# Performance work log

Hardware: AMD Instinct MI355X
Metric: run time of the kernel (lower is better)

## Reference

```python
import jax, jax.numpy as jnp
import numpy as np

N_NEURONS = 50000
N_EDGES = 1600000
EMB_DIM = 2
HID = 128


def _mlp3(x, w0, b0, w1, b1, w2, b2):
    # 3-layer MLP with tanh activations between linear layers (tanh MLP_activation)
    h = jnp.tanh(x @ w0 + b0)
    h = jnp.tanh(h @ w1 + b1)
    return h @ w2 + b2


def setup_inputs() -> dict:
    key = jax.random.key(0)
    ks = jax.random.split(key, 16)
    v = jax.random.normal(ks[0], (N_NEURONS, 1), dtype=jnp.float32)
    excitation = jax.random.uniform(ks[1], (N_NEURONS, 1), dtype=jnp.float32)
    edge_src = jax.random.randint(ks[2], (N_EDGES,), 0, N_NEURONS)
    edge_dst = jax.random.randint(ks[3], (N_EDGES,), 0, N_NEURONS)
    # learnable node embedding a (init ones in torch code; use ones + small noise for generality)
    a = jnp.ones((N_NEURONS, EMB_DIM), jnp.float32) + 0.01 * jax.random.normal(ks[4], (N_NEURONS, EMB_DIM), dtype=jnp.float32)
    # per-edge connectivity W, shape (E, 1) (w_init_mode='randn_scaled')
    W = jax.random.normal(ks[5], (N_EDGES, 1), dtype=jnp.float32) / np.sqrt(N_EDGES).astype(np.float32)
    def lin(k, fan_in, fan_out):
        bound = 1.0 / np.sqrt(fan_in)
        kw, kb = jax.random.split(k)
        w = jax.random.uniform(kw, (fan_in, fan_out), jnp.float32, -bound, bound)
        b = jax.random.uniform(kb, (fan_out,), jnp.float32, -bound, bound)
        return w, b
    # g_phi: input (v_j, a_j) -> 3 dims -> HID -> HID -> 1
    g0_w, g0_b = lin(ks[6], 1 + EMB_DIM, HID)
    g1_w, g1_b = lin(ks[7], HID, HID)
    g2_w, g2_b = lin(ks[8], HID, 1)
    # f_theta: input (v, a, msg, excitation) -> 5 dims -> HID -> HID -> 1
    f0_w, f0_b = lin(ks[9], 1 + EMB_DIM + 1 + 1, HID)
    f1_w, f1_b = lin(ks[10], HID, HID)
    f2_w, f2_b = lin(ks[11], HID, 1)
    return {"v": v, "excitation": excitation, "edge_src": edge_src, "edge_dst": edge_dst,
            "a": a, "W": W,
            "g0_w": g0_w, "g0_b": g0_b, "g1_w": g1_w, "g1_b": g1_b, "g2_w": g2_w, "g2_b": g2_b,
            "f0_w": f0_w, "f0_b": f0_b, "f1_w": f1_w, "f1_b": f1_b, "f2_w": f2_w, "f2_b": f2_b}


def reference(v, excitation, edge_src, edge_dst, a, W,
              g0_w, g0_b, g1_w, g1_b, g2_w, g2_b,
              f0_w, f0_b, f1_w, f1_b, f2_w, f2_b):
    # --- edge messages (flyvis_A): msg_e = W[e] * g_phi(v_src, a_src)^2 ---
    edge_in = jnp.concatenate([v[edge_src], a[edge_src]], axis=1)          # (E, 3)
    g = _mlp3(edge_in, g0_w, g0_b, g1_w, g1_b, g2_w, g2_b)                 # (E, 1)
    msg_e = W * jnp.square(g)                                              # (E, 1), g_phi_positive
    # --- scatter_add aggregation into destination nodes ---
    msg = jax.ops.segment_sum(msg_e, edge_dst, num_segments=N_NEURONS)     # (N, 1)
    # --- node update: du/dt = f_theta(v, a, msg, excitation) ---
    node_in = jnp.concatenate([v, a, msg, excitation], axis=1)             # (N, 5)
    dudt = _mlp3(node_in, f0_w, f0_b, f1_w, f1_b, f2_w, f2_b)              # (N, 1)
    return dudt
```

## Files before the change

### kernel.cpp

```cpp
#include <hip/hip_runtime.h>
#include <hip/hip_bf16.h>

#define HID   128
#define NPB   64
#define PITCH 136
#define CH0   32768

#define FRAGN 16384

typedef float f32x4  __attribute__((ext_vector_type(4)));
typedef short bf16x8 __attribute__((ext_vector_type(8)));

__device__ __forceinline__ float fast_tanh(float x) {
    const float e = __expf(2.0f * x);
    return 1.0f - 2.0f / (e + 1.0f);
}

__device__ __forceinline__ short f2bf(float x) {
    union { __hip_bfloat16 h; short s; } u;
    u.h = __float2bfloat16(x);
    return u.s;
}

__global__ __launch_bounds__(256) void prep_kernel(
    const float* __restrict__ g1_w, const float* __restrict__ g1_b, const float* __restrict__ g2_w,
    const float* __restrict__ f1_w, const float* __restrict__ f1_b, const float* __restrict__ f2_w,
    short* __restrict__ gfrag, short* __restrict__ ffrag,
    float* __restrict__ gbw, float* __restrict__ fbw)
{
    const int id  = blockIdx.x * 256 + threadIdx.x;
    const int mat = (id >= 2560);
    const int r   = id - (mat ? 2560 : 0);
    const float* __restrict__ w1 = mat ? f1_w : g1_w;
    const float* __restrict__ b1 = mat ? f1_b : g1_b;
    const float* __restrict__ w2 = mat ? f2_w : g2_w;
    short* __restrict__ frag = mat ? ffrag : gfrag;
    float* __restrict__ bw   = mat ? fbw   : gbw;

    if (r < 2048) {
        const int j16  = r >> 8;
        const int s    = (r >> 6) & 3;
        const int lane = r & 63;
        const int m = lane & 15, kg = lane >> 4;
        const int j  = j16 * 16 + m;
        const int k0 = 32 * s + 8 * kg;
        bf16x8 f;
#pragma unroll
        for (int e = 0; e < 8; ++e) f[e] = f2bf(w1[(k0 + e) * HID + j]);
        *(bf16x8*)&frag[r * 8] = f;
    } else if (r < 2560) {
        const int q = r - 2048;
        const int j16 = q >> 6, lane = q & 63, kg = lane >> 4;
#pragma unroll
        for (int rr = 0; rr < 4; ++rr) {
            bw[q * 8 + rr]     = b1[j16 * 16 + 4 * kg + rr];
            bw[q * 8 + 4 + rr] = w2[j16 * 16 + 4 * kg + rr];
        }
    }
}

__global__ __launch_bounds__(256) void node_g_kernel(
    const float* __restrict__ v, const float* __restrict__ a,
    const float* __restrict__ g0_w, const float* __restrict__ g0_b,
    const short* __restrict__ gfrag, const float* __restrict__ gbw,
    const float* __restrict__ g2_b,
    float* __restrict__ gsq, int N)
{
    const int t    = threadIdx.x;
    const int lane = t & 63;
    const int wq   = t >> 6;
    const int base = blockIdx.x * NPB;
    const int m    = lane & 15;
    const int kg   = lane >> 4;

    __shared__ __align__(16) __hip_bfloat16 h0bf[NPB * PITCH];
    __shared__ float xv[NPB];
    __shared__ float xa[2 * NPB];
    __shared__ float red[4][4][16];

    if (t < NPB) {
        int node = base + t; if (node >= N) node = N - 1;
        xv[t] = v[node];
    } else if (t >= 128) {
        int idx = 2 * base + (t - 128);
        const int lim = 2 * N - 1; if (idx > lim) idx = lim;
        xa[t - 128] = a[idx];
    }

    bf16x8 afrag[2][4];
    float b1v[2][4], w2v[2][4];
    const bf16x8* __restrict__ fb = (const bf16x8*)gfrag;
#pragma unroll
    for (int jt = 0; jt < 2; ++jt) {
        const int j16 = 2 * wq + jt;
#pragma unroll
        for (int s = 0; s < 4; ++s)
            afrag[jt][s] = fb[(j16 * 4 + s) * 64 + lane];
        const f32x4 bv = *(const f32x4*)&gbw[(j16 * 64 + lane) * 8];
        const f32x4 wv = *(const f32x4*)&gbw[(j16 * 64 + lane) * 8 + 4];
#pragma unroll
        for (int r = 0; r < 4; ++r) { b1v[jt][r] = bv[r]; w2v[jt][r] = wv[r]; }
    }
    __syncthreads();

    {
        const int j    = t & 127;
        const int half = t >> 7;
        const float w00 = g0_w[0 * HID + j];
        const float w01 = g0_w[1 * HID + j];
        const float w02 = g0_w[2 * HID + j];
        const float b0  = g0_b[j];
#pragma unroll 4
        for (int i = 0; i < 32; ++i) {
            const int nn = half * 32 + i;
            h0bf[nn * PITCH + j] = __float2bfloat16(
                fast_tanh(b0 + xv[nn] * w00 + xa[2 * nn] * w01 + xa[2 * nn + 1] * w02));
        }
    }
    __syncthreads();

#pragma unroll
    for (int nt = 0; nt < 4; ++nt) {
        const int n = nt * 16 + m;
        f32x4 acc0 = {0.f, 0.f, 0.f, 0.f};
        f32x4 acc1 = {0.f, 0.f, 0.f, 0.f};
#pragma unroll
        for (int s = 0; s < 4; ++s) {
            const bf16x8 b = *(const bf16x8*)&h0bf[n * PITCH + 32 * s + 8 * kg];
            acc0 = __builtin_amdgcn_mfma_f32_16x16x32_bf16(afrag[0][s], b, acc0, 0, 0, 0);
            acc1 = __builtin_amdgcn_mfma_f32_16x16x32_bf16(afrag[1][s], b, acc1, 0, 0, 0);
        }
        float p = 0.f;
#pragma unroll
        for (int r = 0; r < 4; ++r) {
            p += w2v[0][r] * fast_tanh(acc0[r] + b1v[0][r]);
            p += w2v[1][r] * fast_tanh(acc1[r] + b1v[1][r]);
        }
        p += __shfl_down(p, 32);
        p += __shfl_down(p, 16);
        if (lane < 16) red[wq][nt][lane] = p;
    }
    __syncthreads();

    if (t < NPB) {
        const int node = base + t;
        if (node < N) {
            const float g = red[0][t >> 4][t & 15] + red[1][t >> 4][t & 15]
                          + red[2][t >> 4][t & 15] + red[3][t >> 4][t & 15]
                          + g2_b[0];
            gsq[node] = g * g;
        }
    }
}

__global__ __launch_bounds__(256) void edge_kernel(
    const int* __restrict__ src, const int* __restrict__ dst,
    const float* __restrict__ W, const float* __restrict__ gsq,
    float* __restrict__ partial, int B, int N, int E)
{
    __shared__ float loc[CH0];
    const int t = threadIdx.x;
    const int p = blockIdx.x >> 1;
    const int c = blockIdx.x & 1;

    const f32x4 z4 = {0.f, 0.f, 0.f, 0.f};
    for (int i = 4 * t; i < CH0; i += 1024) *(f32x4*)&loc[i] = z4;
    __syncthreads();

    int cnt = (E + B - 1) / B;
    cnt = (cnt + 3) & ~3;
    const int start = p * cnt;
    int end = start + cnt; if (end > E) end = E;
    const int coff = c << 15;

    if (start < end) {
        const int nvec = (end - start) & ~3;
        for (int i = 4 * t; i < nvec; i += 1024) {
            const int e = start + i;
            const int4   s4 = *(const int4*)&src[e];
            const int4   d4 = *(const int4*)&dst[e];
            const float4 w4 = *(const float4*)&W[e];
            if ((d4.x >> 15) == c) atomicAdd(&loc[d4.x - coff], w4.x * gsq[s4.x]);
            if ((d4.y >> 15) == c) atomicAdd(&loc[d4.y - coff], w4.y * gsq[s4.y]);
            if ((d4.z >> 15) == c) atomicAdd(&loc[d4.z - coff], w4.z * gsq[s4.z]);
            if ((d4.w >> 15) == c) atomicAdd(&loc[d4.w - coff], w4.w * gsq[s4.w]);
        }
        for (int e = start + nvec + t; e < end; e += 256) {
            const int d = dst[e];
            if ((d >> 15) == c) atomicAdd(&loc[d - coff], W[e] * gsq[src[e]]);
        }
    }
    __syncthreads();

    int chN = c ? (N - CH0) : CH0; if (chN > CH0) chN = CH0;
    float* __restrict__ dp = partial + (size_t)p * N + coff;
    const int chV = chN & ~3;
    for (int i = 4 * t; i < chV; i += 1024) *(f32x4*)&dp[i] = *(const f32x4*)&loc[i];
    for (int i = chV + t; i < chN; i += 256) dp[i] = loc[i];
}

__global__ __launch_bounds__(256) void node_f_kernel(
    const float* __restrict__ v, const float* __restrict__ a,
    const float* __restrict__ exc, const float* __restrict__ partial, int B,
    const float* __restrict__ f0_w, const float* __restrict__ f0_b,
    const short* __restrict__ ffrag, const float* __restrict__ fbw,
    const float* __restrict__ f2_b,
    float* __restrict__ out, int N)
{
    const int t    = threadIdx.x;
    const int lane = t & 63;
    const int wq   = t >> 6;
    const int base = blockIdx.x * NPB;
    const int m    = lane & 15;
    const int kg   = lane >> 4;

    __shared__ __align__(16) __hip_bfloat16 h0bf[NPB * PITCH];
    __shared__ float xv[NPB];
    __shared__ float xe[NPB];
    __shared__ float xa[2 * NPB];
    __shared__ float xm4[4][NPB];
    __shared__ float red[4][4][16];

    if (t < NPB) {
        int node = base + t; if (node >= N) node = N - 1;
        xv[t] = v[node];
    } else if (t < 128) {
        int node = base + (t - 64); if (node >= N) node = N - 1;
        xe[t - 64] = exc[node];
    } else {
        int idx = 2 * base + (t - 128);
        const int lim = 2 * N - 1; if (idx > lim) idx = lim;
        xa[t - 128] = a[idx];
    }
    {
        const int n16 = t & 63, grp = t >> 6;
        int node = base + n16; if (node >= N) node = N - 1;
        const int pb = B >> 2;
        float s = 0.f;
        for (int p = grp * pb; p < (grp + 1) * pb; ++p)
            s += partial[(size_t)p * N + node];
        xm4[grp][n16] = s;
    }

    bf16x8 afrag[2][4];
    float b1v[2][4], w2v[2][4];
    const bf16x8* __restrict__ fb = (const bf16x8*)ffrag;
#pragma unroll
    for (int jt = 0; jt < 2; ++jt) {
        const int j16 = 2 * wq + jt;
#pragma unroll
        for (int s = 0; s < 4; ++s)
            afrag[jt][s] = fb[(j16 * 4 + s) * 64 + lane];
        const f32x4 bv = *(const f32x4*)&fbw[(j16 * 64 + lane) * 8];
        const f32x4 wv = *(const f32x4*)&fbw[(j16 * 64 + lane) * 8 + 4];
#pragma unroll
        for (int r = 0; r < 4; ++r) { b1v[jt][r] = bv[r]; w2v[jt][r] = wv[r]; }
    }
    __syncthreads();

    {
        const int j    = t & 127;
        const int half = t >> 7;
        const float w00 = f0_w[0 * HID + j];
        const float w01 = f0_w[1 * HID + j];
        const float w02 = f0_w[2 * HID + j];
        const float w03 = f0_w[3 * HID + j];
        const float w04 = f0_w[4 * HID + j];
        const float b0  = f0_b[j];
#pragma unroll 4
        for (int i = 0; i < 32; ++i) {
            const int nn = half * 32 + i;
            const float x3 = (xm4[0][nn] + xm4[1][nn]) + (xm4[2][nn] + xm4[3][nn]);
            h0bf[nn * PITCH + j] = __float2bfloat16(
                fast_tanh(b0 + xv[nn] * w00 + xa[2 * nn] * w01 + xa[2 * nn + 1] * w02
                             + x3 * w03 + xe[nn] * w04));
        }
    }
    __syncthreads();

#pragma unroll
    for (int nt = 0; nt < 4; ++nt) {
        const int n = nt * 16 + m;
        f32x4 acc0 = {0.f, 0.f, 0.f, 0.f};
        f32x4 acc1 = {0.f, 0.f, 0.f, 0.f};
#pragma unroll
        for (int s = 0; s < 4; ++s) {
            const bf16x8 b = *(const bf16x8*)&h0bf[n * PITCH + 32 * s + 8 * kg];
            acc0 = __builtin_amdgcn_mfma_f32_16x16x32_bf16(afrag[0][s], b, acc0, 0, 0, 0);
            acc1 = __builtin_amdgcn_mfma_f32_16x16x32_bf16(afrag[1][s], b, acc1, 0, 0, 0);
        }
        float p = 0.f;
#pragma unroll
        for (int r = 0; r < 4; ++r) {
            p += w2v[0][r] * fast_tanh(acc0[r] + b1v[0][r]);
            p += w2v[1][r] * fast_tanh(acc1[r] + b1v[1][r]);
        }
        p += __shfl_down(p, 32);
        p += __shfl_down(p, 16);
        if (lane < 16) red[wq][nt][lane] = p;
    }
    __syncthreads();

    if (t < NPB) {
        const int node = base + t;
        if (node < N) {
            out[node] = red[0][t >> 4][t & 15] + red[1][t >> 4][t & 15]
                      + red[2][t >> 4][t & 15] + red[3][t >> 4][t & 15]
                      + f2_b[0];
        }
    }
}

extern "C" void kernel_launch(void* const* d_in, const int* in_sizes, int n_in,
                              void* d_out, int out_size, void* d_ws, size_t ws_size,
                              hipStream_t stream)
{
    const float* v    = (const float*)d_in[0];
    const float* exc  = (const float*)d_in[1];
    const int*   esrc = (const int*)d_in[2];
    const int*   edst = (const int*)d_in[3];
    const float* a    = (const float*)d_in[4];
    const float* W    = (const float*)d_in[5];
    const float* g0_w = (const float*)d_in[6];
    const float* g0_b = (const float*)d_in[7];
    const float* g1_w = (const float*)d_in[8];
    const float* g1_b = (const float*)d_in[9];
    const float* g2_w = (const float*)d_in[10];
    const float* g2_b = (const float*)d_in[11];
    const float* f0_w = (const float*)d_in[12];
    const float* f0_b = (const float*)d_in[13];
    const float* f1_w = (const float*)d_in[14];
    const float* f1_b = (const float*)d_in[15];
    const float* f2_w = (const float*)d_in[16];
    const float* f2_b = (const float*)d_in[17];

    const int N = in_sizes[0];
    const int E = in_sizes[2];

    int B = 128;
    while (B > 4 && (size_t)(1 + B) * (size_t)N * sizeof(float) + 131072 > ws_size) B >>= 1;

    float* gsq     = (float*)d_ws;
    float* partial = gsq + N;
    short* gfrag   = (short*)(partial + (size_t)B * N);
    short* ffrag   = gfrag + FRAGN;
    float* gbw     = (float*)(ffrag + FRAGN);
    float* fbw     = gbw + 4096;

    const int nblocks = (N + NPB - 1) / NPB;

    prep_kernel<<<20, 256, 0, stream>>>(g1_w, g1_b, g2_w, f1_w, f1_b, f2_w,
                                        gfrag, ffrag, gbw, fbw);

    node_g_kernel<<<nblocks, 256, 0, stream>>>(v, a, g0_w, g0_b,
                                               gfrag, gbw, g2_b, gsq, N);

    edge_kernel<<<2 * B, 256, 0, stream>>>(esrc, edst, W, gsq, partial, B, N, E);

    node_f_kernel<<<nblocks, 256, 0, stream>>>(v, a, exc, partial, B,
                                               f0_w, f0_b, ffrag, fbw, f2_b,
                                               (float*)d_out, N);
}
```

Measured before the change: 157.1 us.

## Fuse all four stages into one cooperative persistent kernel with grid syncs

```diff
diff --git a/kernel.cpp b/kernel.cpp
--- a/kernel.cpp
+++ b/kernel.cpp
@@ -1,12 +1,17 @@
 #include <hip/hip_runtime.h>
 #include <hip/hip_bf16.h>
-
-#define HID   128
-#define NPB   64
-#define PITCH 136
-#define CH0   32768
-
-#define FRAGN 16384
+#include <hip/hip_cooperative_groups.h>
+
+namespace cg = cooperative_groups;
+
+#define HID    128
+#define NPB    64
+#define PITCH  136
+#define CH0    32768
+#define BLOCKS 256
+#define TPB    1024
+#define BPARTS 128
+#define FRAGN  16384
 
 typedef float f32x4  __attribute__((ext_vector_type(4)));
 typedef short bf16x8 __attribute__((ext_vector_type(8)));
@@ -15,298 +20,295 @@
     const float e = __expf(2.0f * x);
     return 1.0f - 2.0f / (e + 1.0f);
 }
-
 __device__ __forceinline__ short f2bf(float x) {
     union { __hip_bfloat16 h; short s; } u;
     u.h = __float2bfloat16(x);
     return u.s;
 }
 
-__global__ __launch_bounds__(256) void prep_kernel(
-    const float* __restrict__ g1_w, const float* __restrict__ g1_b, const float* __restrict__ g2_w,
-    const float* __restrict__ f1_w, const float* __restrict__ f1_b, const float* __restrict__ f2_w,
-    short* __restrict__ gfrag, short* __restrict__ ffrag,
-    float* __restrict__ gbw, float* __restrict__ fbw)
+__global__ __launch_bounds__(TPB) void fused_kernel(
+    const float* __restrict__ v, const float* __restrict__ exc,
+    const int* __restrict__ esrc, const int* __restrict__ edst,
+    const float* __restrict__ a, const float* __restrict__ W,
+    const float* __restrict__ g0_w, const float* __restrict__ g0_b,
+    const float* __restrict__ g1_w, const float* __restrict__ g1_b,
+    const float* __restrict__ g2_w, const float* __restrict__ g2_b,
+    const float* __restrict__ f0_w, const float* __restrict__ f0_b,
+    const float* __restrict__ f1_w, const float* __restrict__ f1_b,
+    const float* __restrict__ f2_w, const float* __restrict__ f2_b,
+    float* __restrict__ out, float* __restrict__ ws, int N, int E)
 {
-    const int id  = blockIdx.x * 256 + threadIdx.x;
-    const int mat = (id >= 2560);
-    const int r   = id - (mat ? 2560 : 0);
-    const float* __restrict__ w1 = mat ? f1_w : g1_w;
-    const float* __restrict__ b1 = mat ? f1_b : g1_b;
-    const float* __restrict__ w2 = mat ? f2_w : g2_w;
-    short* __restrict__ frag = mat ? ffrag : gfrag;
-    float* __restrict__ bw   = mat ? fbw   : gbw;
-
-    if (r < 2048) {
-        const int j16  = r >> 8;
-        const int s    = (r >> 6) & 3;
-        const int lane = r & 63;
-        const int m = lane & 15, kg = lane >> 4;
-        const int j  = j16 * 16 + m;
-        const int k0 = 32 * s + 8 * kg;
-        bf16x8 f;
-#pragma unroll
-        for (int e = 0; e < 8; ++e) f[e] = f2bf(w1[(k0 + e) * HID + j]);
-        *(bf16x8*)&frag[r * 8] = f;
-    } else if (r < 2560) {
-        const int q = r - 2048;
-        const int j16 = q >> 6, lane = q & 63, kg = lane >> 4;
-#pragma unroll
-        for (int rr = 0; rr < 4; ++rr) {
-            bw[q * 8 + rr]     = b1[j16 * 16 + 4 * kg + rr];
-            bw[q * 8 + 4 + rr] = w2[j16 * 16 + 4 * kg + rr];
-        }
-    }
-}
-
-__global__ __launch_bounds__(256) void node_g_kernel(
-    const float* __restrict__ v, const float* __restrict__ a,
-    const float* __restrict__ g0_w, const float* __restrict__ g0_b,
-    const short* __restrict__ gfrag, const float* __restrict__ gbw,
-    const float* __restrict__ g2_b,
-    float* __restrict__ gsq, int N)
-{
-    const int t    = threadIdx.x;
+    float* gsq     = ws;
+    float* partial = ws + N;
+    short* gfrag   = (short*)(partial + (size_t)BPARTS * N);
+    short* ffrag   = gfrag + FRAGN;
+    float* gbw     = (float*)(ffrag + FRAGN);
+    float* fbw     = gbw + 4096;
+
+    cg::grid_group grid = cg::this_grid();
+
+    __shared__ __align__(16) char lds[131072];
+
+    const int tid  = threadIdx.x;
+    const int team = tid >> 8;
+    const int t    = tid & 255;
     const int lane = t & 63;
     const int wq   = t >> 6;
-    const int base = blockIdx.x * NPB;
     const int m    = lane & 15;
     const int kg   = lane >> 4;
-
-    __shared__ __align__(16) __hip_bfloat16 h0bf[NPB * PITCH];
-    __shared__ float xv[NPB];
-    __shared__ float xa[2 * NPB];
-    __shared__ float red[4][4][16];
-
-    if (t < NPB) {
-        int node = base + t; if (node >= N) node = N - 1;
-        xv[t] = v[node];
-    } else if (t >= 128) {
-        int idx = 2 * base + (t - 128);
-        const int lim = 2 * N - 1; if (idx > lim) idx = lim;
-        xa[t - 128] = a[idx];
+    const int tile = blockIdx.x * 4 + team;
+    const int base = tile * NPB;
+
+    char* tb = lds + team * 32768;
+    __hip_bfloat16* h0bf = (__hip_bfloat16*)tb;
+    float* xv  = (float*)(tb + 17408);
+    float* xa  = (float*)(tb + 17664);
+    float* xe  = (float*)(tb + 18176);
+    float* xm4 = (float*)(tb + 18432);
+    float* red = (float*)(tb + 19456);
+
+    {
+        const int id = blockIdx.x * TPB + tid;
+        if (id < 5120) {
+            const int mat = (id >= 2560);
+            const int r   = id - (mat ? 2560 : 0);
+            const float* __restrict__ w1 = mat ? f1_w : g1_w;
+            const float* __restrict__ b1 = mat ? f1_b : g1_b;
+            const float* __restrict__ w2 = mat ? f2_w : g2_w;
+            short* __restrict__ frag = mat ? ffrag : gfrag;
+            float* __restrict__ bw   = mat ? fbw   : gbw;
+            if (r < 2048) {
+                const int j16 = r >> 8, s = (r >> 6) & 3, ln = r & 63;
+                const int mm = ln & 15, kk = ln >> 4;
+                const int j = j16 * 16 + mm, k0 = 32 * s + 8 * kk;
+                bf16x8 f;
+#pragma unroll
+                for (int e = 0; e < 8; ++e) f[e] = f2bf(w1[(k0 + e) * HID + j]);
+                *(bf16x8*)&frag[r * 8] = f;
+            } else if (r < 2560) {
+                const int q = r - 2048;
+                const int j16 = q >> 6, ln = q & 63, kk = ln >> 4;
+#pragma unroll
+                for (int rr = 0; rr < 4; ++rr) {
+                    bw[q * 8 + rr]     = b1[j16 * 16 + 4 * kk + rr];
+                    bw[q * 8 + 4 + rr] = w2[j16 * 16 + 4 * kk + rr];
+                }
+            }
+        }
     }
-
-    bf16x8 afrag[2][4];
-    float b1v[2][4], w2v[2][4];
-    const bf16x8* __restrict__ fb = (const bf16x8*)gfrag;
-#pragma unroll
-    for (int jt = 0; jt < 2; ++jt) {
-        const int j16 = 2 * wq + jt;
-#pragma unroll
-        for (int s = 0; s < 4; ++s)
-            afrag[jt][s] = fb[(j16 * 4 + s) * 64 + lane];
-        const f32x4 bv = *(const f32x4*)&gbw[(j16 * 64 + lane) * 8];
-        const f32x4 wv = *(const f32x4*)&gbw[(j16 * 64 + lane) * 8 + 4];
-#pragma unroll
-        for (int r = 0; r < 4; ++r) { b1v[jt][r] = bv[r]; w2v[jt][r] = wv[r]; }
+    grid.sync();
+
+    {
+        if (t < NPB) {
+            int node = base + t; if (node >= N) node = N - 1;
+            xv[t] = v[node];
+        } else if (t >= 128) {
+            int idx = 2 * base + (t - 128);
+            const int lim = 2 * N - 1; if (idx > lim) idx = lim;
+            xa[t - 128] = a[idx];
+        }
+
+        bf16x8 afrag[2][4];
+        float b1v[2][4], w2v[2][4];
+        const bf16x8* __restrict__ fb = (const bf16x8*)gfrag;
+#pragma unroll
+        for (int jt = 0; jt < 2; ++jt) {
+            const int j16 = 2 * wq + jt;
+#pragma unroll
+            for (int s = 0; s < 4; ++s)
+                afrag[jt][s] = fb[(j16 * 4 + s) * 64 + lane];
+            const f32x4 bv = *(const f32x4*)&gbw[(j16 * 64 + lane) * 8];
+            const f32x4 wv = *(const f32x4*)&gbw[(j16 * 64 + lane) * 8 + 4];
+#pragma unroll
+            for (int r = 0; r < 4; ++r) { b1v[jt][r] = bv[r]; w2v[jt][r] = wv[r]; }
+        }
+        __syncthreads();
+
+        {
+            const int j    = t & 127;
+            const int half = t >> 7;
+            const float w00 = g0_w[0 * HID + j];
+            const float w01 = g0_w[1 * HID + j];
+            const float w02 = g0_w[2 * HID + j];
+            const float b0  = g0_b[j];
+#pragma unroll 4
+            for (int i = 0; i < 32; ++i) {
+                const int nn = half * 32 + i;
+                h0bf[nn * PITCH + j] = __float2bfloat16(
+                    fast_tanh(b0 + xv[nn] * w00 + xa[2 * nn] * w01 + xa[2 * nn + 1] * w02));
+            }
+        }
+        __syncthreads();
+
+#pragma unroll
+        for (int nt = 0; nt < 4; ++nt) {
+            const int n = nt * 16 + m;
+            f32x4 acc0 = {0.f, 0.f, 0.f, 0.f};
+            f32x4 acc1 = {0.f, 0.f, 0.f, 0.f};
+#pragma unroll
+            for (int s = 0; s < 4; ++s) {
+                const bf16x8 b = *(const bf16x8*)&h0bf[n * PITCH + 32 * s + 8 * kg];
+                acc0 = __builtin_amdgcn_mfma_f32_16x16x32_bf16(afrag[0][s], b, acc0, 0, 0, 0);
+                acc1 = __builtin_amdgcn_mfma_f32_16x16x32_bf16(afrag[1][s], b, acc1, 0, 0, 0);
+            }
+            float p = 0.f;
+#pragma unroll
+            for (int r = 0; r < 4; ++r) {
+                p += w2v[0][r] * fast_tanh(acc0[r] + b1v[0][r]);
+                p += w2v[1][r] * fast_tanh(acc1[r] + b1v[1][r]);
+            }
+            p += __shfl_down(p, 32);
+            p += __shfl_down(p, 16);
+            if (lane < 16) red[(wq * 4 + nt) * 16 + lane] = p;
+        }
+        __syncthreads();
+
+        if (t < NPB) {
+            const int node = base + t;
+            if (node < N) {
+                const int nt = t >> 4, n16 = t & 15;
+                const float g = red[(0 * 4 + nt) * 16 + n16] + red[(1 * 4 + nt) * 16 + n16]
+                              + red[(2 * 4 + nt) * 16 + n16] + red[(3 * 4 + nt) * 16 + n16]
+                              + g2_b[0];
+                gsq[node] = g * g;
+            }
+        }
     }
-    __syncthreads();
+    grid.sync();
 
     {
-        const int j    = t & 127;
-        const int half = t >> 7;
-        const float w00 = g0_w[0 * HID + j];
-        const float w01 = g0_w[1 * HID + j];
-        const float w02 = g0_w[2 * HID + j];
-        const float b0  = g0_b[j];
+        float* __restrict__ loc = (float*)lds;
+        const int p = blockIdx.x >> 1;
+        const int c = blockIdx.x & 1;
+
+        const f32x4 z4 = {0.f, 0.f, 0.f, 0.f};
+        for (int i = 4 * tid; i < CH0; i += 4 * TPB) *(f32x4*)&loc[i] = z4;
+        __syncthreads();
+
+        int cnt = (E + BPARTS - 1) / BPARTS;
+        cnt = (cnt + 3) & ~3;
+        const int start = p * cnt;
+        int end = start + cnt; if (end > E) end = E;
+        const int coff = c << 15;
+
+        if (start < end) {
+            const int nvec = (end - start) & ~3;
+            for (int i = 4 * tid; i < nvec; i += 4 * TPB) {
+                const int e = start + i;
+                const int4   s4 = *(const int4*)&esrc[e];
+                const int4   d4 = *(const int4*)&edst[e];
+                const float4 w4 = *(const float4*)&W[e];
+                if ((d4.x >> 15) == c) atomicAdd(&loc[d4.x - coff], w4.x * gsq[s4.x]);
+                if ((d4.y >> 15) == c) atomicAdd(&loc[d4.y - coff], w4.y * gsq[s4.y]);
+                if ((d4.z >> 15) == c) atomicAdd(&loc[d4.z - coff], w4.z * gsq[s4.z]);
+                if ((d4.w >> 15) == c) atomicAdd(&loc[d4.w - coff], w4.w * gsq[s4.w]);
+            }
+            for (int e = start + nvec + tid; e < end; e += TPB) {
+                const int d = edst[e];
+                if ((d >> 15) == c) atomicAdd(&loc[d - coff], W[e] * gsq[esrc[e]]);
+            }
+        }
+        __syncthreads();
+
+        int chN = c ? (N - CH0) : CH0;
+        if (chN > CH0) chN = CH0; if (chN < 0) chN = 0;
+        float* __restrict__ dp = partial + (size_t)p * N + coff;
+        const int chV = chN & ~3;
+        for (int i = 4 * tid; i < chV; i += 4 * TPB) *(f32x4*)&dp[i] = *(const f32x4*)&loc[i];
+        for (int i = chV + tid; i < chN; i += TPB) dp[i] = loc[i];
+    }
+    grid.sync();
+
+    {
+        if (t < NPB) {
+            int node = base + t; if (node >= N) node = N - 1;
+            xv[t] = v[node];
+        } else if (t < 128) {
+            int node = base + (t - 64); if (node >= N) node = N - 1;
+            xe[t - 64] = exc[node];
+        } else {
+            int idx = 2 * base + (t - 128);
+            const int lim = 2 * N - 1; if (idx > lim) idx = lim;
+            xa[t - 128] = a[idx];
+        }
+        {
+            const int n16 = t & 63, grp = t >> 6;
+            int node = base + n16; if (node >= N) node = N - 1;
+            const int pb = BPARTS >> 2;
+            float s = 0.f;
+            for (int p = grp * pb; p < (grp + 1) * pb; ++p)
+                s += partial[(size_t)p * N + node];
+            xm4[grp * NPB + n16] = s;
+        }
+
+        bf16x8 afrag[2][4];
+        float b1v[2][4], w2v[2][4];
+        const bf16x8* __restrict__ fb = (const bf16x8*)ffrag;
+#pragma unroll
+        for (int jt = 0; jt < 2; ++jt) {
+            const int j16 = 2 * wq + jt;
+#pragma unroll
+            for (int s = 0; s < 4; ++s)
+                afrag[jt][s] = fb[(j16 * 4 + s) * 64 + lane];
+            const f32x4 bv = *(const f32x4*)&fbw[(j16 * 64 + lane) * 8];
+            const f32x4 wv = *(const f32x4*)&fbw[(j16 * 64 + lane) * 8 + 4];
+#pragma unroll
+            for (int r = 0; r < 4; ++r) { b1v[jt][r] = bv[r]; w2v[jt][r] = wv[r]; }
+        }
+        __syncthreads();
+
+        {
+            const int j    = t & 127;
+            const int half = t >> 7;
+            const float w00 = f0_w[0 * HID + j];
+            const float w01 = f0_w[1 * HID + j];
+            const float w02 = f0_w[2 * HID + j];
+            const float w03 = f0_w[3 * HID + j];
+            const float w04 = f0_w[4 * HID + j];
+            const float b0  = f0_b[j];
 #pragma unroll 4
-        for (int i = 0; i < 32; ++i) {
-            const int nn = half * 32 + i;
-            h0bf[nn * PITCH + j] = __float2bfloat16(
-                fast_tanh(b0 + xv[nn] * w00 + xa[2 * nn] * w01 + xa[2 * nn + 1] * w02));
-        }
-    }
-    __syncthreads();
-
-#pragma unroll
-    for (int nt = 0; nt < 4; ++nt) {
-        const int n = nt * 16 + m;
-        f32x4 acc0 = {0.f, 0.f, 0.f, 0.f};
-        f32x4 acc1 = {0.f, 0.f, 0.f, 0.f};
-#pragma unroll
-        for (int s = 0; s < 4; ++s) {
-            const bf16x8 b = *(const bf16x8*)&h0bf[n * PITCH + 32 * s + 8 * kg];
-            acc0 = __builtin_amdgcn_mfma_f32_16x16x32_bf16(afrag[0][s], b, acc0, 0, 0, 0);
-            acc1 = __builtin_amdgcn_mfma_f32_16x16x32_bf16(afrag[1][s], b, acc1, 0, 0, 0);
-        }
-        float p = 0.f;
-#pragma unroll
-        for (int r = 0; r < 4; ++r) {
-            p += w2v[0][r] * fast_tanh(acc0[r] + b1v[0][r]);
-            p += w2v[1][r] * fast_tanh(acc1[r] + b1v[1][r]);
-        }
-        p += __shfl_down(p, 32);
-        p += __shfl_down(p, 16);
-        if (lane < 16) red[wq][nt][lane] = p;
-    }
-    __syncthreads();
-
-    if (t < NPB) {
-        const int node = base + t;
-        if (node < N) {
-            const float g = red[0][t >> 4][t & 15] + red[1][t >> 4][t & 15]
-                          + red[2][t >> 4][t & 15] + red[3][t >> 4][t & 15]
-                          + g2_b[0];
-            gsq[node] = g * g;
-        }
-    }
-}
-
-__global__ __launch_bounds__(256) void edge_kernel(
-    const int* __restrict__ src, const int* __restrict__ dst,
-    const float* __restrict__ W, const float* __restrict__ gsq,
-    float* __restrict__ partial, int B, int N, int E)
-{
-    __shared__ float loc[CH0];
-    const int t = threadIdx.x;
-    const int p = blockIdx.x >> 1;
-    const int c = blockIdx.x & 1;
-
-    const f32x4 z4 = {0.f, 0.f, 0.f, 0.f};
-    for (int i = 4 * t; i < CH0; i += 1024) *(f32x4*)&loc[i] = z4;
-    __syncthreads();
-
-    int cnt = (E + B - 1) / B;
-    cnt = (cnt + 3) & ~3;
-    const int start = p * cnt;
-    int end = start + cnt; if (end > E) end = E;
-    const int coff = c << 15;
-
-    if (start < end) {
-        const int nvec = (end - start) & ~3;
-        for (int i = 4 * t; i < nvec; i += 1024) {
-            const int e = start + i;
-            const int4   s4 = *(const int4*)&src[e];
-            const int4   d4 = *(const int4*)&dst[e];
-            const float4 w4 = *(const float4*)&W[e];
-            if ((d4.x >> 15) == c) atomicAdd(&loc[d4.x - coff], w4.x * gsq[s4.x]);
-            if ((d4.y >> 15) == c) atomicAdd(&loc[d4.y - coff], w4.y * gsq[s4.y]);
-            if ((d4.z >> 15) == c) atomicAdd(&loc[d4.z - coff], w4.z * gsq[s4.z]);
-            if ((d4.w >> 15) == c) atomicAdd(&loc[d4.w - coff], w4.w * gsq[s4.w]);
-        }
-        for (int e = start + nvec + t; e < end; e += 256) {
-            const int d = dst[e];
-            if ((d >> 15) == c) atomicAdd(&loc[d - coff], W[e] * gsq[src[e]]);
-        }
-    }
-    __syncthreads();
-
-    int chN = c ? (N - CH0) : CH0; if (chN > CH0) chN = CH0;
-    float* __restrict__ dp = partial + (size_t)p * N + coff;
-    const int chV = chN & ~3;
-    for (int i = 4 * t; i < chV; i += 1024) *(f32x4*)&dp[i] = *(const f32x4*)&loc[i];
-    for (int i = chV + t; i < chN; i += 256) dp[i] = loc[i];
-}
-
-__global__ __launch_bounds__(256) void node_f_kernel(
-    const float* __restrict__ v, const float* __restrict__ a,
-    const float* __restrict__ exc, const float* __restrict__ partial, int B,
-    const float* __restrict__ f0_w, const float* __restrict__ f0_b,
-    const short* __restrict__ ffrag, const float* __restrict__ fbw,
-    const float* __restrict__ f2_b,
-    float* __restrict__ out, int N)
-{
-    const int t    = threadIdx.x;
-    const int lane = t & 63;
-    const int wq   = t >> 6;
-    const int base = blockIdx.x * NPB;
-    const int m    = lane & 15;
-    const int kg   = lane >> 4;
-
-    __shared__ __align__(16) __hip_bfloat16 h0bf[NPB * PITCH];
-    __shared__ float xv[NPB];
-    __shared__ float xe[NPB];
-    __shared__ float xa[2 * NPB];
-    __shared__ float xm4[4][NPB];
-    __shared__ float red[4][4][16];
-
-    if (t < NPB) {
-        int node = base + t; if (node >= N) node = N - 1;
-        xv[t] = v[node];
-    } else if (t < 128) {
-        int node = base + (t - 64); if (node >= N) node = N - 1;
-        xe[t - 64] = exc[node];
-    } else {
-        int idx = 2 * base + (t - 128);
-        const int lim = 2 * N - 1; if (idx > lim) idx = lim;
-        xa[t - 128] = a[idx];
-    }
-    {
-        const int n16 = t & 63, grp = t >> 6;
-        int node = base + n16; if (node >= N) node = N - 1;
-        const int pb = B >> 2;
-        float s = 0.f;
-        for (int p = grp * pb; p < (grp + 1) * pb; ++p)
-            s += partial[(size_t)p * N + node];
-        xm4[grp][n16] = s;
-    }
-
-    bf16x8 afrag[2][4];
-    float b1v[2][4], w2v[2][4];
-    const bf16x8* __restrict__ fb = (const bf16x8*)ffrag;
-#pragma unroll
-    for (int jt = 0; jt < 2; ++jt) {
-        const int j16 = 2 * wq + jt;
-#pragma unroll
-        for (int s = 0; s < 4; ++s)
-            afrag[jt][s] = fb[(j16 * 4 + s) * 64 + lane];
-        const f32x4 bv = *(const f32x4*)&fbw[(j16 * 64 + lane) * 8];
-        const f32x4 wv = *(const f32x4*)&fbw[(j16 * 64 + lane) * 8 + 4];
-#pragma unroll
-        for (int r = 0; r < 4; ++r) { b1v[jt][r] = bv[r]; w2v[jt][r] = wv[r]; }
-    }
-    __syncthreads();
-
-    {
-        const int j    = t & 127;
-        const int half = t >> 7;
-        const float w00 = f0_w[0 * HID + j];
-        const float w01 = f0_w[1 * HID + j];
-        const float w02 = f0_w[2 * HID + j];
-        const float w03 = f0_w[3 * HID + j];
-        const float w04 = f0_w[4 * HID + j];
-        const float b0  = f0_b[j];
-#pragma unroll 4
-        for (int i = 0; i < 32; ++i) {
-            const int nn = half * 32 + i;
-            const float x3 = (xm4[0][nn] + xm4[1][nn]) + (xm4[2][nn] + xm4[3][nn]);
-            h0bf[nn * PITCH + j] = __float2bfloat16(
-                fast_tanh(b0 + xv[nn] * w00 + xa[2 * nn] * w01 + xa[2 * nn + 1] * w02
-                             + x3 * w03 + xe[nn] * w04));
-        }
-    }
-    __syncthreads();
-
-#pragma unroll
-    for (int nt = 0; nt < 4; ++nt) {
-        const int n = nt * 16 + m;
-        f32x4 acc0 = {0.f, 0.f, 0.f, 0.f};
-        f32x4 acc1 = {0.f, 0.f, 0.f, 0.f};
-#pragma unroll
-        for (int s = 0; s < 4; ++s) {
-            const bf16x8 b = *(const bf16x8*)&h0bf[n * PITCH + 32 * s + 8 * kg];
-            acc0 = __builtin_amdgcn_mfma_f32_16x16x32_bf16(afrag[0][s], b, acc0, 0, 0, 0);
-            acc1 = __builtin_amdgcn_mfma_f32_16x16x32_bf16(afrag[1][s], b, acc1, 0, 0, 0);
-        }
-        float p = 0.f;
-#pragma unroll
-        for (int r = 0; r < 4; ++r) {
-            p += w2v[0][r] * fast_tanh(acc0[r] + b1v[0][r]);
-            p += w2v[1][r] * fast_tanh(acc1[r] + b1v[1][r]);
-        }
-        p += __shfl_down(p, 32);
-        p += __shfl_down(p, 16);
-        if (lane < 16) red[wq][nt][lane] = p;
-    }
-    __syncthreads();
-
-    if (t < NPB) {
-        const int node = base + t;
-        if (node < N) {
-            out[node] = red[0][t >> 4][t & 15] + red[1][t >> 4][t & 15]
-                      + red[2][t >> 4][t & 15] + red[3][t >> 4][t & 15]
-                      + f2_b[0];
+            for (int i = 0; i < 32; ++i) {
+                const int nn = half * 32 + i;
+                const float x3 = (xm4[0 * NPB + nn] + xm4[1 * NPB + nn])
+                               + (xm4[2 * NPB + nn] + xm4[3 * NPB + nn]);
+                h0bf[nn * PITCH + j] = __float2bfloat16(
+                    fast_tanh(b0 + xv[nn] * w00 + xa[2 * nn] * w01 + xa[2 * nn + 1] * w02
+                                 + x3 * w03 + xe[nn] * w04));
+            }
+        }
+        __syncthreads();
+
+#pragma unroll
+        for (int nt = 0; nt < 4; ++nt) {
+            const int n = nt * 16 + m;
+            f32x4 acc0 = {0.f, 0.f, 0.f, 0.f};
+            f32x4 acc1 = {0.f, 0.f, 0.f, 0.f};
+#pragma unroll
+            for (int s = 0; s < 4; ++s) {
+                const bf16x8 b = *(const bf16x8*)&h0bf[n * PITCH + 32 * s + 8 * kg];
+                acc0 = __builtin_amdgcn_mfma_f32_16x16x32_bf16(afrag[0][s], b, acc0, 0, 0, 0);
+                acc1 = __builtin_amdgcn_mfma_f32_16x16x32_bf16(afrag[1][s], b, acc1, 0, 0, 0);
+            }
+            float p = 0.f;
+#pragma unroll
+            for (int r = 0; r < 4; ++r) {
+                p += w2v[0][r] * fast_tanh(acc0[r] + b1v[0][r]);
+                p += w2v[1][r] * fast_tanh(acc1[r] + b1v[1][r]);
+            }
+            p += __shfl_down(p, 32);
+            p += __shfl_down(p, 16);
+            if (lane < 16) red[(wq * 4 + nt) * 16 + lane] = p;
+        }
+        __syncthreads();
+
+        if (t < NPB) {
+            const int node = base + t;
+            if (node < N) {
+                const int nt = t >> 4, n16 = t & 15;
+                out[node] = red[(0 * 4 + nt) * 16 + n16] + red[(1 * 4 + nt) * 16 + n16]
+                          + red[(2 * 4 + nt) * 16 + n16] + red[(3 * 4 + nt) * 16 + n16]
+                          + f2_b[0];
+            }
         }
     }
 }
@@ -334,30 +336,20 @@
     const float* f2_w = (const float*)d_in[16];
     const float* f2_b = (const float*)d_in[17];
 
-    const int N = in_sizes[0];
-    const int E = in_sizes[2];
-
-    int B = 128;
-    while (B > 4 && (size_t)(1 + B) * (size_t)N * sizeof(float) + 131072 > ws_size) B >>= 1;
-
-    float* gsq     = (float*)d_ws;
-    float* partial = gsq + N;
-    short* gfrag   = (short*)(partial + (size_t)B * N);
-    short* ffrag   = gfrag + FRAGN;
-    float* gbw     = (float*)(ffrag + FRAGN);
-    float* fbw     = gbw + 4096;
-
-    const int nblocks = (N + NPB - 1) / NPB;
-
-    prep_kernel<<<20, 256, 0, stream>>>(g1_w, g1_b, g2_w, f1_w, f1_b, f2_w,
-                                        gfrag, ffrag, gbw, fbw);
-
-    node_g_kernel<<<nblocks, 256, 0, stream>>>(v, a, g0_w, g0_b,
-                                               gfrag, gbw, g2_b, gsq, N);
-
-    edge_kernel<<<2 * B, 256, 0, stream>>>(esrc, edst, W, gsq, partial, B, N, E);
-
-    node_f_kernel<<<nblocks, 256, 0, stream>>>(v, a, exc, partial, B,
-                                               f0_w, f0_b, ffrag, fbw, f2_b,
-                                               (float*)d_out, N);
+    int N = in_sizes[0];
+    int E = in_sizes[2];
+
+    float* ws   = (float*)d_ws;
+    float* outp = (float*)d_out;
+
+    void* args[] = { (void*)&v, (void*)&exc, (void*)&esrc, (void*)&edst,
+                     (void*)&a, (void*)&W,
+                     (void*)&g0_w, (void*)&g0_b, (void*)&g1_w, (void*)&g1_b,
+                     (void*)&g2_w, (void*)&g2_b,
+                     (void*)&f0_w, (void*)&f0_b, (void*)&f1_w, (void*)&f1_b,
+                     (void*)&f2_w, (void*)&f2_b,
+                     (void*)&outp, (void*)&ws, (void*)&N, (void*)&E };
+
+    hipLaunchCooperativeKernel((const void*)fused_kernel,
+                               dim3(BLOCKS), dim3(TPB), args, 0, stream);
 }
```

Result: slower. 255.2 us (+62.5%).
